# Performance work log

Measured on AMD Instinct MI355X. Metric: run time of the kernel, lower is better.

The kernel has to match this reference:

```python
import jax, jax.numpy as jnp
import numpy as np

T, S, B, D, H, DH, DI = 1024, 1024, 4, 1024, 16, 64, 4096
SCALE = 1.0 / (DH ** 0.5)


def _ln(x, g, b, eps=1e-5):
    m = jnp.mean(x, axis=-1, keepdims=True)
    v = jnp.mean((x - m) ** 2, axis=-1, keepdims=True)
    return (x - m) * jax.lax.rsqrt(v + eps) * g + b


def setup_inputs() -> dict:
    key = jax.random.key(0)
    ks = jax.random.split(key, 16)
    s = 0.02
    inp = {
        "dec_inp": jax.random.normal(ks[0], (T, B, D), jnp.float32),
        "enc_out": jax.random.normal(ks[1], (T, B, D), jnp.float32),
        # causal mask for self-attn: [qlen, klen, bsz], True = masked
        "dec_mask": jnp.broadcast_to(jnp.triu(jnp.ones((T, T), bool), 1)[:, :, None], (T, T, B)),
        # encoder padding mask: [klen, bsz], last 128 positions padded
        "enc_mask": jnp.broadcast_to((jnp.arange(S) >= S - 128)[:, None], (S, B)),
        # self-attn params
        "W_q1": jax.random.normal(ks[2], (D, H * DH), jnp.float32) * s,
        "W_kv1": jax.random.normal(ks[3], (D, 2 * H * DH), jnp.float32) * s,
        "W_o1": jax.random.normal(ks[4], (H * DH, D), jnp.float32) * s,
        "g1": jnp.ones((D,), jnp.float32), "b1": jnp.zeros((D,), jnp.float32),
        # cross-attn params
        "W_q2": jax.random.normal(ks[5], (D, H * DH), jnp.float32) * s,
        "W_kv2": jax.random.normal(ks[6], (D, 2 * H * DH), jnp.float32) * s,
        "W_o2": jax.random.normal(ks[7], (H * DH, D), jnp.float32) * s,
        "g2": jnp.ones((D,), jnp.float32), "b2": jnp.zeros((D,), jnp.float32),
        # FFN params
        "W_ff1": jax.random.normal(ks[8], (D, DI), jnp.float32) * s,
        "b_ff1": jnp.zeros((DI,), jnp.float32),
        "W_ff2": jax.random.normal(ks[9], (DI, D), jnp.float32) * s,
        "b_ff2": jnp.zeros((D,), jnp.float32),
        "g3": jnp.ones((D,), jnp.float32), "b3": jnp.zeros((D,), jnp.float32),
    }
    return inp


def reference(dec_inp, enc_out, dec_mask, enc_mask,
              W_q1, W_kv1, W_o1, g1, b1,
              W_q2, W_kv2, W_o2, g2, b2,
              W_ff1, b_ff1, W_ff2, b_ff2, g3, b3):
    # ---- self-attention (MultiHeadAttn, pre_lnorm=True, mems=None) ----
    # NOTE: q is computed from the UN-normalized h; k,v from LN(c) — faithful to source.
    c = _ln(dec_inp, g1, b1)
    q = (dec_inp @ W_q1).reshape(T, B, H, DH)
    kv = (c @ W_kv1)
    k, v = jnp.split(kv, 2, axis=-1)
    k = k.reshape(T, B, H, DH)
    v = v.reshape(T, B, H, DH)
    score = jnp.einsum('ibnd,jbnd->ijbn', q, k) * SCALE  # [T,T,B,H]
    score = jnp.where(dec_mask[:, :, :, None], -jnp.inf, score)
    prob = jax.nn.softmax(score, axis=1)
    vec = jnp.einsum('ijbn,jbnd->ibnd', prob, v).reshape(T, B, H * DH)
    out1 = dec_inp + vec @ W_o1

    # ---- cross-attention (ContextMultiHeadAttn, pre_lnorm=True) ----
    # NOTE: residual uses the layer-normed h (source reassigns h = layer_norm(h)).
    h2 = _ln(out1, g2, b2)
    q2 = (h2 @ W_q2).reshape(T, B, H, DH)
    kv2 = enc_out @ W_kv2  # enc_out is NOT layer-normed in source
    k2, v2 = jnp.split(kv2, 2, axis=-1)
    k2 = k2.reshape(S, B, H, DH)
    v2 = v2.reshape(S, B, H, DH)
    score2 = jnp.einsum('ibnd,jbnd->ijbn', q2, k2) * SCALE  # [T,S,B,H]
    score2 = jnp.where(enc_mask[None, :, :, None], -10000.0, score2)
    prob2 = jax.nn.softmax(score2, axis=1)
    vec2 = jnp.einsum('ijbn,jbnd->ibnd', prob2, v2).reshape(T, B, H * DH)
    out2 = h2 + vec2 @ W_o2

    # ---- position-wise FFN (pre_lnorm) ----
    h3 = _ln(out2, g3, b3)
    core = jax.nn.gelu(h3 @ W_ff1 + b_ff1, approximate=False) @ W_ff2 + b_ff2
    return out2 + core
```

## Files before the change

kernel.cpp:

```cpp
#include <hip/hip_runtime.h>
#include <hip/hip_bf16.h>

#define T_ 1024
#define S_ 1024
#define B_ 4
#define D_ 1024
#define H_ 16
#define DH_ 64
#define DI_ 4096
#define NTOK 4096

typedef __attribute__((ext_vector_type(8))) short bf16x8;
typedef __attribute__((ext_vector_type(4))) float f32x4;

__device__ __forceinline__ short f2bf(float f) {
  unsigned u = __builtin_bit_cast(unsigned, f);
  u += 0x7fffu + ((u >> 16) & 1u);
  return (short)(u >> 16);
}

__device__ __forceinline__ void g2l16(const void* g, void* l) {
  __builtin_amdgcn_global_load_lds(
      (const __attribute__((address_space(1))) unsigned int*)g,
      (__attribute__((address_space(3))) unsigned int*)l, 16, 0, 0);
}

__device__ __forceinline__ void bar() {
  asm volatile("" ::: "memory");
  __builtin_amdgcn_s_barrier();
  asm volatile("" ::: "memory");
}

__device__ __forceinline__ void xcd_swz(int& bx, int& by) {
  const int gx = gridDim.x;
  const int id0 = blockIdx.y * gx + blockIdx.x;
  const int cpx = (gx * gridDim.y) >> 3;
  const int nid = (id0 & 7) * cpx + (id0 >> 3);
  bx = nid % gx;
  by = nid / gx;
}

template <int EPI>
__global__ __launch_bounds__(512, 2) void gemm8p(
    const short* __restrict__ A, const short* __restrict__ Bt,
    float* __restrict__ outF, short* __restrict__ outB,
    const float* __restrict__ res, const float* __restrict__ bias,
    int M, int N, int K) {
  __shared__ short sA[2][256 * 64];
  __shared__ short sB[2][256 * 64];
  const int tid = threadIdx.x;
  const int lane = tid & 63;
  const int w = tid >> 6;
  const int wm = w >> 2, wn = w & 3;
  const int r15 = lane & 15, g4 = lane >> 4;
  int bx, by;
  xcd_swz(bx, by);
  const size_t row0 = (size_t)bx * 256;
  const size_t col0 = (size_t)by * 256;

  f32x4 acc[8][4];
#pragma unroll
  for (int i = 0; i < 8; i++)
#pragma unroll
    for (int j = 0; j < 4; j++) acc[i][j] = (f32x4){0.f, 0.f, 0.f, 0.f};

  auto stageA = [&](int buf, int s, int kt) {
    const int k0 = kt << 6;
#pragma unroll
    for (int j = 0; j < 2; ++j) {
      const int c = j * 8 + w;
      const int rb = ((c >> 3) << 7) + (s << 6) + ((c & 7) << 3);
      const int row = rb + (lane >> 3);
      const int col = k0 + (((lane & 7) ^ (row & 7)) << 3);
      g2l16(A + (row0 + row) * (size_t)K + col, &sA[buf][rb * 64]);
    }
  };
  auto stageB = [&](int buf, int s, int kt) {
    const int k0 = kt << 6;
#pragma unroll
    for (int j = 0; j < 2; ++j) {
      const int c = j * 8 + w;
      const int rb = ((c >> 2) << 6) + (s << 5) + ((c & 3) << 3);
      const int row = rb + (lane >> 3);
      const int col = k0 + (((lane & 7) ^ (row & 7)) << 3);
      g2l16(Bt + (col0 + row) * (size_t)K + col, &sB[buf][rb * 64]);
    }
  };

  const int nk = K >> 6;
  stageA(0, 0, 0); stageA(0, 1, 0); stageB(0, 0, 0); stageB(0, 1, 0);
  if (nk > 1) {
    stageA(1, 0, 1); stageB(1, 1, 1);
    asm volatile("s_waitcnt vmcnt(4)" ::: "memory");
  } else {
    asm volatile("s_waitcnt vmcnt(0)" ::: "memory");
  }
  bar();

  bf16x8 af[4][2], bv[2][2];
  for (int t = 0; t < nk; ++t) {
    const int cur = t & 1;
    const short* cA = sA[cur];
    const short* cB = sB[cur];
#pragma unroll
    for (int mi = 0; mi < 4; mi++) {
      const int rowA = wm * 128 + mi * 16 + r15;
#pragma unroll
      for (int kk = 0; kk < 2; kk++)
        af[mi][kk] = *(const bf16x8*)(cA + rowA * 64 +
                                      (((kk * 4 + g4) ^ (rowA & 7)) << 3));
    }
#pragma unroll
    for (int ni = 0; ni < 2; ni++) {
      const int rowB = wn * 64 + ni * 16 + r15;
#pragma unroll
      for (int kk = 0; kk < 2; kk++)
        bv[ni][kk] = *(const bf16x8*)(cB + rowB * 64 +
                                      (((kk * 4 + g4) ^ (rowB & 7)) << 3));
    }
    if (t + 1 < nk) stageA(cur ^ 1, 1, t + 1);
    bar();
    asm volatile("s_waitcnt lgkmcnt(0)" ::: "memory");
    __builtin_amdgcn_s_setprio(1);
#pragma unroll
    for (int kk = 0; kk < 2; kk++)
#pragma unroll
      for (int mi = 0; mi < 4; mi++)
#pragma unroll
        for (int ni = 0; ni < 2; ni++)
          acc[mi][ni] = __builtin_amdgcn_mfma_f32_16x16x32_bf16(
              af[mi][kk], bv[ni][kk], acc[mi][ni], 0, 0, 0);
    __builtin_amdgcn_s_setprio(0);
    bar();
#pragma unroll
    for (int ni = 0; ni < 2; ni++) {
      const int rowB = wn * 64 + (2 + ni) * 16 + r15;
#pragma unroll
      for (int kk = 0; kk < 2; kk++)
        bv[ni][kk] = *(const bf16x8*)(cB + rowB * 64 +
                                      (((kk * 4 + g4) ^ (rowB & 7)) << 3));
    }
    if (t + 1 < nk) stageB(cur ^ 1, 0, t + 1);
    bar();
    asm volatile("s_waitcnt lgkmcnt(0)" ::: "memory");
    __builtin_amdgcn_s_setprio(1);
#pragma unroll
    for (int kk = 0; kk < 2; kk++)
#pragma unroll
      for (int mi = 0; mi < 4; mi++)
#pragma unroll
        for (int ni = 0; ni < 2; ni++)
          acc[mi][2 + ni] = __builtin_amdgcn_mfma_f32_16x16x32_bf16(
              af[mi][kk], bv[ni][kk], acc[mi][2 + ni], 0, 0, 0);
    __builtin_amdgcn_s_setprio(0);
    bar();
#pragma unroll
    for (int mi = 0; mi < 4; mi++) {
      const int rowA = wm * 128 + (4 + mi) * 16 + r15;
#pragma unroll
      for (int kk = 0; kk < 2; kk++)
        af[mi][kk] = *(const bf16x8*)(cA + rowA * 64 +
                                      (((kk * 4 + g4) ^ (rowA & 7)) << 3));
    }
    if (t + 2 < nk) stageA(cur, 0, t + 2);
    bar();
    asm volatile("s_waitcnt lgkmcnt(0)" ::: "memory");
    __builtin_amdgcn_s_setprio(1);
#pragma unroll
    for (int kk = 0; kk < 2; kk++)
#pragma unroll
      for (int mi = 0; mi < 4; mi++)
#pragma unroll
        for (int ni = 0; ni < 2; ni++)
          acc[4 + mi][2 + ni] = __builtin_amdgcn_mfma_f32_16x16x32_bf16(
              af[mi][kk], bv[ni][kk], acc[4 + mi][2 + ni], 0, 0, 0);
    __builtin_amdgcn_s_setprio(0);
    bar();
#pragma unroll
    for (int ni = 0; ni < 2; ni++) {
      const int rowB = wn * 64 + ni * 16 + r15;
#pragma unroll
      for (int kk = 0; kk < 2; kk++)
        bv[ni][kk] = *(const bf16x8*)(cB + rowB * 64 +
                                      (((kk * 4 + g4) ^ (rowB & 7)) << 3));
    }
    if (t + 2 < nk) stageB(cur, 1, t + 2);
    bar();
    asm volatile("s_waitcnt lgkmcnt(0)" ::: "memory");
    __builtin_amdgcn_s_setprio(1);
#pragma unroll
    for (int kk = 0; kk < 2; kk++)
#pragma unroll
      for (int mi = 0; mi < 4; mi++)
#pragma unroll
        for (int ni = 0; ni < 2; ni++)
          acc[4 + mi][ni] = __builtin_amdgcn_mfma_f32_16x16x32_bf16(
              af[mi][kk], bv[ni][kk], acc[4 + mi][ni], 0, 0, 0);
    __builtin_amdgcn_s_setprio(0);
    if (t + 2 < nk)
      asm volatile("s_waitcnt vmcnt(4)" ::: "memory");
    else if (t + 1 < nk)
      asm volatile("s_waitcnt vmcnt(0)" ::: "memory");
    bar();
  }

#pragma unroll
  for (int mi = 0; mi < 8; mi++) {
    size_t row = row0 + wm * 128 + mi * 16 + (g4 << 2);
#pragma unroll
    for (int ni = 0; ni < 4; ni++) {
      size_t col = col0 + wn * 64 + ni * 16 + r15;
      float bcol = (EPI == 2 || EPI == 3) ? bias[col] : 0.f;
#pragma unroll
      for (int r = 0; r < 4; r++) {
        size_t idx = (row + r) * (size_t)N + col;
        float v = acc[mi][ni][r];
        if (EPI == 0) {
          outB[idx] = f2bf(v);
        } else if (EPI == 1) {
          outF[idx] = v + res[idx];
        } else if (EPI == 2) {
          float x = v + bcol;
          float gl = 0.5f * x * (1.f + erff(x * 0.70710678118654752f));
          outB[idx] = f2bf(gl);
        } else {
          outF[idx] = v + bcol + res[idx];
        }
      }
    }
  }
}

template <int EPI, int BN>
__global__ __launch_bounds__(256, 2) void gemm_bt(
    const short* __restrict__ A, const short* __restrict__ Bt,
    float* __restrict__ outF, short* __restrict__ outB,
    const float* __restrict__ res, const float* __restrict__ bias,
    short* __restrict__ Kgp, short* __restrict__ Vgp,
    int M, int N, int K) {
  constexpr int WCOLS = BN / 64;
  constexpr int MI = (WCOLS == 2) ? 4 : 2;
  constexpr int BLOADS = BN / 32;
  __shared__ short sA[2][128 * 64];
  __shared__ short sB[2][BN * 64];
  const int tid = threadIdx.x;
  const int lane = tid & 63;
  const int w = tid >> 6;
  const int wr = (WCOLS == 2) ? (w >> 1) : w;
  const int wc = (WCOLS == 2) ? (w & 1) : 0;
  const int r15 = lane & 15, g4 = lane >> 4;
  int bx, by;
  xcd_swz(bx, by);
  const size_t row0 = (size_t)bx * 128;
  const size_t col0 = (size_t)by * BN;

  f32x4 acc[MI][4];
#pragma unroll
  for (int i = 0; i < MI; i++)
#pragma unroll
    for (int j = 0; j < 4; j++) acc[i][j] = (f32x4){0.f, 0.f, 0.f, 0.f};

  auto stage = [&](int buf, int kt) {
    const int k0 = kt << 6;
#pragma unroll
    for (int i = 0; i < 4; i++) {
      int flat = i * 256 + tid;
      int row = flat >> 3;
      int col = k0 + (((flat & 7) ^ (row & 7)) << 3);
      g2l16(A + (row0 + row) * (size_t)K + col, &sA[buf][(i * 256 + w * 64) * 8]);
    }
#pragma unroll
    for (int i = 0; i < BLOADS; i++) {
      int flat = i * 256 + tid;
      int row = flat >> 3;
      int col = k0 + (((flat & 7) ^ (row & 7)) << 3);
      g2l16(Bt + (col0 + row) * (size_t)K + col, &sB[buf][(i * 256 + w * 64) * 8]);
    }
  };

  stage(0, 0);
  __syncthreads();

  const int nk = K >> 6;
  for (int kt = 0; kt < nk; ++kt) {
    const int cur = kt & 1;
    if (kt + 1 < nk) stage(cur ^ 1, kt + 1);
#pragma unroll
    for (int kk = 0; kk < 2; ++kk) {
      bf16x8 af[MI], bfr[4];
#pragma unroll
      for (int mi = 0; mi < MI; mi++) {
        int rowA = wr * (MI * 16) + mi * 16 + r15;
        af[mi] = *(const bf16x8*)(&sA[cur][rowA * 64 +
                                           (((kk * 4 + g4) ^ (rowA & 7)) << 3)]);
      }
#pragma unroll
      for (int ni = 0; ni < 4; ni++) {
        int rowB = wc * 64 + ni * 16 + r15;
        bfr[ni] = *(const bf16x8*)(&sB[cur][rowB * 64 +
                                            (((kk * 4 + g4) ^ (rowB & 7)) << 3)]);
      }
#pragma unroll
      for (int mi = 0; mi < MI; mi++)
#pragma unroll
        for (int ni = 0; ni < 4; ni++)
          acc[mi][ni] = __builtin_amdgcn_mfma_f32_16x16x32_bf16(af[mi], bfr[ni],
                                                                acc[mi][ni], 0, 0, 0);
    }
    __syncthreads();
  }

#pragma unroll
  for (int mi = 0; mi < MI; mi++) {
    size_t row = row0 + wr * (MI * 16) + mi * 16 + (g4 << 2);
#pragma unroll
    for (int ni = 0; ni < 4; ni++) {
      size_t col = col0 + wc * 64 + ni * 16 + r15;
      float bcol = (EPI == 2 || EPI == 3) ? bias[col] : 0.f;
#pragma unroll
      for (int r = 0; r < 4; r++) {
        size_t idx = (row + r) * (size_t)N + col;
        float v = acc[mi][ni][r];
        if (EPI == 0) {
          outB[idx] = f2bf(v);
        } else if (EPI == 1) {
          outF[idx] = v + res[idx];
        } else if (EPI == 2) {
          float x = v + bcol;
          float gl = 0.5f * x * (1.f + erff(x * 0.70710678118654752f));
          outB[idx] = f2bf(gl);
        } else if (EPI == 3) {
          outF[idx] = v + bcol + res[idx];
        } else {
          int tt = (int)(row + r) >> 2;
          int bb = (int)(row + r) & 3;
          int cc = (int)col;
          if (cc < 1024) {
            int hh = cc >> 6, dd = cc & 63;
            size_t base = (size_t)(bb * 16 + hh) * 65536 + (size_t)tt * 64;
            Kgp[base + ((((dd >> 3) ^ (tt & 7)) << 3) | (dd & 7))] = f2bf(v * 0.125f);
          } else {
            int hh = (cc >> 6) - 16, dd = cc & 63;
            int k6 = tt & 63;
            int kap = ((k6 & 15) << 2) | (k6 >> 4);
            size_t base = (size_t)(bb * 16 + hh) * 65536 + (size_t)(tt >> 6) * 4096;
            Vgp[base + (kap >> 3) * 512 + dd * 8 + (kap & 7)] = f2bf(v);
          }
        }
      }
    }
  }
}

template <int MODE>
__global__ __launch_bounds__(256, 3) void attn_k2(const short* __restrict__ Qm,
                                                  const short* __restrict__ Kg,
                                                  const short* __restrict__ Vg,
                                                  short* __restrict__ Om) {
  __shared__ short Kl[2][4096];
  __shared__ short Vl[2][4096];
  __shared__ short Pl[4][2048];
  const int tid = threadIdx.x;
  const int lane = tid & 63;
  const int w = tid >> 6;
  const int r15 = lane & 15, g4 = lane >> 4;
  const int bh = blockIdx.x;
  const int qt = blockIdx.y;
  const int b = bh >> 4, h = bh & 15;
  const int qbase = qt * 128 + w * 32;
  const int ktDiag = qbase >> 6;

  bf16x8 qf[2][2];
#pragma unroll
  for (int g = 0; g < 2; g++)
#pragma unroll
    for (int hf = 0; hf < 2; hf++) {
      int row = qbase + g * 16 + r15;
      qf[g][hf] = *(const bf16x8*)(Qm + ((size_t)(row * 4 + b)) * 1024 + h * 64 +
                                   hf * 32 + g4 * 8);
    }

  const size_t kvbase = (size_t)bh * 65536;
  const int nkt = (MODE == 0) ? (2 * qt + 2) : 14;

  f32x4 o[2][4];
#pragma unroll
  for (int g = 0; g < 2; g++)
#pragma unroll
    for (int ni = 0; ni < 4; ni++) o[g][ni] = (f32x4){0.f, 0.f, 0.f, 0.f};
  float mrun[2][4], lrun[2][4];
#pragma unroll
  for (int g = 0; g < 2; g++)
#pragma unroll
    for (int r = 0; r < 4; r++) { mrun[g][r] = -1e30f; lrun[g][r] = 0.f; }

  {
    const size_t tb = kvbase;
#pragma unroll
    for (int i = 0; i < 2; i++) {
      g2l16(Kg + tb + (size_t)(i * 256 + tid) * 8, &Kl[0][(i * 256 + w * 64) * 8]);
      g2l16(Vg + tb + (size_t)(i * 256 + tid) * 8, &Vl[0][(i * 256 + w * 64) * 8]);
    }
  }
  __syncthreads();

  for (int kt = 0; kt < nkt; kt++) {
    const int cur = kt & 1;
    if (kt + 1 < nkt) {
      const size_t tb = kvbase + (size_t)(kt + 1) * 4096;
#pragma unroll
      for (int i = 0; i < 2; i++) {
        g2l16(Kg + tb + (size_t)(i * 256 + tid) * 8,
              &Kl[cur ^ 1][(i * 256 + w * 64) * 8]);
        g2l16(Vg + tb + (size_t)(i * 256 + tid) * 8,
              &Vl[cur ^ 1][(i * 256 + w * 64) * 8]);
      }
    }

    const bool active = (MODE == 1) || (kt * 64 <= qbase + 31);
    if (active) {
      bf16x8 kb[4][2];
#pragma unroll
      for (int ni = 0; ni < 4; ni++) {
        int row = ni * 16 + r15;
        kb[ni][0] = *(const bf16x8*)(&Kl[cur][row * 64 + ((g4 ^ (row & 7)) << 3)]);
        kb[ni][1] =
            *(const bf16x8*)(&Kl[cur][row * 64 + (((g4 + 4) ^ (row & 7)) << 3)]);
      }
      f32x4 sf[2][4];
#pragma unroll
      for (int g = 0; g < 2; g++)
#pragma unroll
        for (int ni = 0; ni < 4; ni++) {
          f32x4 s = (f32x4){0.f, 0.f, 0.f, 0.f};
          s = __builtin_amdgcn_mfma_f32_16x16x32_bf16(qf[g][0], kb[ni][0], s, 0, 0, 0);
          s = __builtin_amdgcn_mfma_f32_16x16x32_bf16(qf[g][1], kb[ni][1], s, 0, 0, 0);
          sf[g][ni] = s;
        }
      if (MODE == 0 && kt >= ktDiag) {
#pragma unroll
        for (int g = 0; g < 2; g++)
#pragma unroll
          for (int ni = 0; ni < 4; ni++)
#pragma unroll
            for (int r = 0; r < 4; r++) {
              int q = qbase + g * 16 + g4 * 4 + r;
              int key = kt * 64 + ni * 16 + r15;
              if (key > q) sf[g][ni][r] = -1e30f;
            }
      }
#pragma unroll
      for (int g = 0; g < 2; g++) {
        float corr[4];
#pragma unroll
        for (int r = 0; r < 4; r++) {
          float m = fmaxf(fmaxf(sf[g][0][r], sf[g][1][r]),
                          fmaxf(sf[g][2][r], sf[g][3][r]));
          m = fmaxf(m, __shfl_xor(m, 1));
          m = fmaxf(m, __shfl_xor(m, 2));
          m = fmaxf(m, __shfl_xor(m, 4));
          m = fmaxf(m, __shfl_xor(m, 8));
          float mn = fmaxf(mrun[g][r], m);
          corr[r] = __expf(mrun[g][r] - mn);
          mrun[g][r] = mn;
        }
        float rs[4] = {0.f, 0.f, 0.f, 0.f};
#pragma unroll
        for (int ni = 0; ni < 4; ni++)
#pragma unroll
          for (int r = 0; r < 4; r++) {
            float p = __expf(sf[g][ni][r] - mrun[g][r]);
            sf[g][ni][r] = p;
            rs[r] += p;
          }
#pragma unroll
        for (int r = 0; r < 4; r++) {
          rs[r] += __shfl_xor(rs[r], 1);
          rs[r] += __shfl_xor(rs[r], 2);
          rs[r] += __shfl_xor(rs[r], 4);
          rs[r] += __shfl_xor(rs[r], 8);
          lrun[g][r] = lrun[g][r] * corr[r] + rs[r];
        }
#pragma unroll
        for (int ni = 0; ni < 4; ni++)
#pragma unroll
          for (int r = 0; r < 4; r++) o[g][ni][r] *= corr[r];
#pragma unroll
        for (int r = 0; r < 4; r++) {
          int qr = g * 16 + g4 * 4 + r;
          short4 pk;
          pk.x = f2bf(sf[g][0][r]);
          pk.y = f2bf(sf[g][1][r]);
          pk.z = f2bf(sf[g][2][r]);
          pk.w = f2bf(sf[g][3][r]);
          int gran = (r15 >> 1) ^ (qr & 7);
          *(short4*)(&Pl[w][qr * 64 + gran * 8 + (r15 & 1) * 4]) = pk;
        }
      }
#pragma unroll
      for (int kk = 0; kk < 2; kk++) {
        int gw = kk * 4 + g4;
        bf16x8 pa0 = *(const bf16x8*)(&Pl[w][r15 * 64 + ((gw ^ (r15 & 7)) << 3)]);
        bf16x8 pa1 =
            *(const bf16x8*)(&Pl[w][(16 + r15) * 64 + ((gw ^ (r15 & 7)) << 3)]);
#pragma unroll
        for (int ni = 0; ni < 4; ni++) {
          bf16x8 vb = *(const bf16x8*)(&Vl[cur][(gw * 64 + ni * 16 + r15) * 8]);
          o[0][ni] = __builtin_amdgcn_mfma_f32_16x16x32_bf16(pa0, vb, o[0][ni], 0, 0, 0);
          o[1][ni] = __builtin_amdgcn_mfma_f32_16x16x32_bf16(pa1, vb, o[1][ni], 0, 0, 0);
        }
      }
    }
    __syncthreads();
  }

#pragma unroll
  for (int g = 0; g < 2; g++) {
    float inv[4];
#pragma unroll
    for (int r = 0; r < 4; r++) inv[r] = 1.f / lrun[g][r];
#pragma unroll
    for (int ni = 0; ni < 4; ni++) {
      int col = h * 64 + ni * 16 + r15;
#pragma unroll
      for (int r = 0; r < 4; r++) {
        int tg = qbase + g * 16 + g4 * 4 + r;
        Om[((size_t)(tg * 4 + b)) * 1024 + col] = f2bf(o[g][ni][r] * inv[r]);
      }
    }
  }
}

__global__ __launch_bounds__(256) void ln_k(const float* __restrict__ x,
                                            const float* __restrict__ gw,
                                            const float* __restrict__ bw,
                                            float* __restrict__ outF,
                                            short* __restrict__ outB,
                                            short* __restrict__ outXB) {
  const int row = blockIdx.x, tid = threadIdx.x;
  const float4 v = ((const float4*)(x + (size_t)row * 1024))[tid];
  float s = v.x + v.y + v.z + v.w;
  float ss = v.x * v.x + v.y * v.y + v.z * v.z + v.w * v.w;
#pragma unroll
  for (int d = 32; d >= 1; d >>= 1) {
    s += __shfl_xor(s, d);
    ss += __shfl_xor(ss, d);
  }
  __shared__ float red[8];
  const int w = tid >> 6;
  if ((tid & 63) == 0) { red[w] = s; red[4 + w] = ss; }
  __syncthreads();
  s = red[0] + red[1] + red[2] + red[3];
  ss = red[4] + red[5] + red[6] + red[7];
  const float mean = s * (1.f / 1024.f);
  const float var = ss * (1.f / 1024.f) - mean * mean;
  const float rstd = rsqrtf(var + 1e-5f);
  const float4 gv = ((const float4*)gw)[tid];
  const float4 bv = ((const float4*)bw)[tid];
  float4 y;
  y.x = (v.x - mean) * rstd * gv.x + bv.x;
  y.y = (v.y - mean) * rstd * gv.y + bv.y;
  y.z = (v.z - mean) * rstd * gv.z + bv.z;
  y.w = (v.w - mean) * rstd * gv.w + bv.w;
  if (outF) ((float4*)(outF + (size_t)row * 1024))[tid] = y;
  if (outB) {
    short4 ob;
    ob.x = f2bf(y.x); ob.y = f2bf(y.y); ob.z = f2bf(y.z); ob.w = f2bf(y.w);
    ((short4*)(outB + (size_t)row * 1024))[tid] = ob;
  }
  if (outXB) {
    short4 ob;
    ob.x = f2bf(v.x); ob.y = f2bf(v.y); ob.z = f2bf(v.z); ob.w = f2bf(v.w);
    ((short4*)(outXB + (size_t)row * 1024))[tid] = ob;
  }
}

__global__ __launch_bounds__(256) void cvt_bf16(const float* __restrict__ in,
                                                short* __restrict__ out) {
  const size_t i = (size_t)blockIdx.x * 256 + threadIdx.x;
  const float4 v = ((const float4*)in)[i];
  short4 ob;
  ob.x = f2bf(v.x); ob.y = f2bf(v.y); ob.z = f2bf(v.z); ob.w = f2bf(v.w);
  ((short4*)out)[i] = ob;
}

__global__ __launch_bounds__(256) void tr_cvt(const float* __restrict__ in,
                                              short* __restrict__ out, int K, int N) {
  __shared__ float t[64][65];
  const int tid = threadIdx.x;
  const int k0 = blockIdx.x * 64, n0 = blockIdx.y * 64;
#pragma unroll
  for (int i = 0; i < 16; i++) {
    int flat = i * 256 + tid;
    int r = flat >> 6, c = flat & 63;
    t[r][c] = in[(size_t)(k0 + r) * N + n0 + c];
  }
  __syncthreads();
#pragma unroll
  for (int i = 0; i < 16; i++) {
    int flat = i * 256 + tid;
    int r = flat >> 6, c = flat & 63;
    out[(size_t)(n0 + r) * K + k0 + c] = f2bf(t[c][r]);
  }
}

extern "C" void kernel_launch(void* const* d_in, const int* in_sizes, int n_in,
                              void* d_out, int out_size, void* d_ws, size_t ws_size,
                              hipStream_t stream) {
  const float* dec_inp = (const float*)d_in[0];
  const float* enc_out = (const float*)d_in[1];
  const float* W_q1 = (const float*)d_in[4];
  const float* W_kv1 = (const float*)d_in[5];
  const float* W_o1 = (const float*)d_in[6];
  const float* g1 = (const float*)d_in[7];
  const float* b1 = (const float*)d_in[8];
  const float* W_q2 = (const float*)d_in[9];
  const float* W_kv2 = (const float*)d_in[10];
  const float* W_o2 = (const float*)d_in[11];
  const float* g2 = (const float*)d_in[12];
  const float* b2 = (const float*)d_in[13];
  const float* W_ff1 = (const float*)d_in[14];
  const float* b_ff1 = (const float*)d_in[15];
  const float* W_ff2 = (const float*)d_in[16];
  const float* b_ff2 = (const float*)d_in[17];
  const float* g3 = (const float*)d_in[18];
  const float* b3 = (const float*)d_in[19];
  float* out = (float*)d_out;

  char* ws = (char*)d_ws;
  size_t off = 0;
  auto alloc = [&](size_t bytes) -> void* {
    void* p = ws + off;
    off += (bytes + 255) & ~(size_t)255;
    return p;
  };
  short* Wq1t = (short*)alloc(1024ull * 1024 * 2);
  short* Wkv1t = (short*)alloc(2048ull * 1024 * 2);
  short* Wo1t = (short*)alloc(1024ull * 1024 * 2);
  short* Wq2t = (short*)alloc(1024ull * 1024 * 2);
  short* Wkv2t = (short*)alloc(2048ull * 1024 * 2);
  short* Wo2t = (short*)alloc(1024ull * 1024 * 2);
  short* Wff1t = (short*)alloc(4096ull * 1024 * 2);
  short* Wff2t = (short*)alloc(1024ull * 4096 * 2);
  short* Xbf = (short*)alloc((size_t)NTOK * 1024 * 2);
  short* Ebf = (short*)alloc((size_t)NTOK * 1024 * 2);
  short* Cbf = (short*)alloc((size_t)NTOK * 1024 * 2);
  short* Qb = (short*)alloc((size_t)NTOK * 1024 * 2);
  short* Kg = (short*)alloc(64ull * 65536 * 2);
  short* Vg = (short*)alloc(64ull * 65536 * 2);
  short* VECb = (short*)alloc((size_t)NTOK * 1024 * 2);
  float* OUT1 = (float*)alloc((size_t)NTOK * 1024 * 4);
  float* H2f = (float*)alloc((size_t)NTOK * 1024 * 4);
  float* OUT2 = (float*)alloc((size_t)NTOK * 1024 * 4);
  short* FF1 = (short*)alloc((size_t)NTOK * 4096 * 2);
  short* H2b = Xbf;
  short* H3b = Cbf;

  dim3 blk(256, 1, 1);

  tr_cvt<<<dim3(16, 16), blk, 0, stream>>>(W_q1, Wq1t, 1024, 1024);
  tr_cvt<<<dim3(16, 32), blk, 0, stream>>>(W_kv1, Wkv1t, 1024, 2048);
  tr_cvt<<<dim3(16, 16), blk, 0, stream>>>(W_o1, Wo1t, 1024, 1024);
  tr_cvt<<<dim3(16, 16), blk, 0, stream>>>(W_q2, Wq2t, 1024, 1024);
  tr_cvt<<<dim3(16, 32), blk, 0, stream>>>(W_kv2, Wkv2t, 1024, 2048);
  tr_cvt<<<dim3(16, 16), blk, 0, stream>>>(W_o2, Wo2t, 1024, 1024);
  tr_cvt<<<dim3(16, 64), blk, 0, stream>>>(W_ff1, Wff1t, 1024, 4096);
  tr_cvt<<<dim3(64, 16), blk, 0, stream>>>(W_ff2, Wff2t, 4096, 1024);

  cvt_bf16<<<4096, blk, 0, stream>>>(enc_out, Ebf);
  ln_k<<<4096, blk, 0, stream>>>(dec_inp, g1, b1, nullptr, Cbf, Xbf);

  gemm_bt<0, 64><<<dim3(32, 16), blk, 0, stream>>>(
      Xbf, Wq1t, nullptr, Qb, nullptr, nullptr, nullptr, nullptr, 4096, 1024, 1024);
  gemm_bt<4, 128><<<dim3(32, 16), blk, 0, stream>>>(
      Cbf, Wkv1t, nullptr, nullptr, nullptr, nullptr, Kg, Vg, 4096, 2048, 1024);
  attn_k2<0><<<dim3(64, 8), blk, 0, stream>>>(Qb, Kg, Vg, VECb);
  gemm_bt<1, 64><<<dim3(32, 16), blk, 0, stream>>>(
      VECb, Wo1t, OUT1, nullptr, dec_inp, nullptr, nullptr, nullptr, 4096, 1024, 1024);
  ln_k<<<4096, blk, 0, stream>>>(OUT1, g2, b2, H2f, H2b, nullptr);
  gemm_bt<0, 64><<<dim3(32, 16), blk, 0, stream>>>(
      H2b, Wq2t, nullptr, Qb, nullptr, nullptr, nullptr, nullptr, 4096, 1024, 1024);
  gemm_bt<4, 128><<<dim3(32, 16), blk, 0, stream>>>(
      Ebf, Wkv2t, nullptr, nullptr, nullptr, nullptr, Kg, Vg, 4096, 2048, 1024);
  attn_k2<1><<<dim3(64, 8), blk, 0, stream>>>(Qb, Kg, Vg, VECb);
  gemm_bt<1, 64><<<dim3(32, 16), blk, 0, stream>>>(
      VECb, Wo2t, OUT2, nullptr, H2f, nullptr, nullptr, nullptr, 4096, 1024, 1024);
  ln_k<<<4096, blk, 0, stream>>>(OUT2, g3, b3, nullptr, H3b, nullptr);
  gemm8p<2><<<dim3(16, 16), dim3(512, 1, 1), 0, stream>>>(
      H3b, Wff1t, nullptr, FF1, nullptr, b_ff1, 4096, 4096, 1024);
  gemm_bt<3, 64><<<dim3(32, 16), blk, 0, stream>>>(
      FF1, Wff2t, out, nullptr, OUT2, b_ff2, nullptr, nullptr, 4096, 1024, 4096);
}
```

Measured before the change: 399.3 us.

## Triple-buffer gemm_bt with single barrier, drop XCD swizzle and BN=128 variant

Rewrites the gemm_bt main loop to a three-stage LDS ring: it prefetches two tiles ahead and uses explicit vmcnt waits with one barrier per k-step instead of two syncthreads. This is meant to hide global-to-LDS latency better. It also removes the XCD block-index swizzle from both GEMM kernels and replaces the BN=128 KV-projection tiles with BN=64 on a doubled grid. Dropping the swizzle can hurt L2 locality across XCDs, and the smaller KV tile reduces reuse of A.

```diff
diff --git a/kernel.cpp b/kernel.cpp
--- a/kernel.cpp
+++ b/kernel.cpp
@@ -29,15 +29,6 @@
   asm volatile("" ::: "memory");
   __builtin_amdgcn_s_barrier();
   asm volatile("" ::: "memory");
-}
-
-__device__ __forceinline__ void xcd_swz(int& bx, int& by) {
-  const int gx = gridDim.x;
-  const int id0 = blockIdx.y * gx + blockIdx.x;
-  const int cpx = (gx * gridDim.y) >> 3;
-  const int nid = (id0 & 7) * cpx + (id0 >> 3);
-  bx = nid % gx;
-  by = nid / gx;
 }
 
 template <int EPI>
@@ -53,10 +44,8 @@
   const int w = tid >> 6;
   const int wm = w >> 2, wn = w & 3;
   const int r15 = lane & 15, g4 = lane >> 4;
-  int bx, by;
-  xcd_swz(bx, by);
-  const size_t row0 = (size_t)bx * 256;
-  const size_t col0 = (size_t)by * 256;
+  const size_t row0 = (size_t)blockIdx.x * 256;
+  const size_t col0 = (size_t)blockIdx.y * 256;
 
   f32x4 acc[8][4];
 #pragma unroll
@@ -231,32 +220,25 @@
   }
 }
 
-template <int EPI, int BN>
+template <int EPI>
 __global__ __launch_bounds__(256, 2) void gemm_bt(
     const short* __restrict__ A, const short* __restrict__ Bt,
     float* __restrict__ outF, short* __restrict__ outB,
     const float* __restrict__ res, const float* __restrict__ bias,
     short* __restrict__ Kgp, short* __restrict__ Vgp,
     int M, int N, int K) {
-  constexpr int WCOLS = BN / 64;
-  constexpr int MI = (WCOLS == 2) ? 4 : 2;
-  constexpr int BLOADS = BN / 32;
-  __shared__ short sA[2][128 * 64];
-  __shared__ short sB[2][BN * 64];
+  __shared__ short sA[3][128 * 64];
+  __shared__ short sB[3][64 * 64];
   const int tid = threadIdx.x;
   const int lane = tid & 63;
   const int w = tid >> 6;
-  const int wr = (WCOLS == 2) ? (w >> 1) : w;
-  const int wc = (WCOLS == 2) ? (w & 1) : 0;
   const int r15 = lane & 15, g4 = lane >> 4;
-  int bx, by;
-  xcd_swz(bx, by);
-  const size_t row0 = (size_t)bx * 128;
-  const size_t col0 = (size_t)by * BN;
-
-  f32x4 acc[MI][4];
-#pragma unroll
-  for (int i = 0; i < MI; i++)
+  const size_t row0 = (size_t)blockIdx.x * 128;
+  const size_t col0 = (size_t)blockIdx.y * 64;
+
+  f32x4 acc[2][4];
+#pragma unroll
+  for (int i = 0; i < 2; i++)
 #pragma unroll
     for (int j = 0; j < 4; j++) acc[i][j] = (f32x4){0.f, 0.f, 0.f, 0.f};
 
@@ -270,7 +252,7 @@
       g2l16(A + (row0 + row) * (size_t)K + col, &sA[buf][(i * 256 + w * 64) * 8]);
     }
 #pragma unroll
-    for (int i = 0; i < BLOADS; i++) {
+    for (int i = 0; i < 2; i++) {
       int flat = i * 256 + tid;
       int row = flat >> 3;
       int col = k0 + (((flat & 7) ^ (row & 7)) << 3);
@@ -278,44 +260,54 @@
     }
   };
 
+  const int nk = K >> 6;
   stage(0, 0);
-  __syncthreads();
-
-  const int nk = K >> 6;
+  stage(1, 1);
+  int cur = 0;
   for (int kt = 0; kt < nk; ++kt) {
-    const int cur = kt & 1;
-    if (kt + 1 < nk) stage(cur ^ 1, kt + 1);
+    if (kt + 1 < nk)
+      asm volatile("s_waitcnt vmcnt(6)" ::: "memory");
+    else
+      asm volatile("s_waitcnt vmcnt(0)" ::: "memory");
+    bar();
+    if (kt + 2 < nk) {
+      int nxt = cur + 2;
+      if (nxt >= 3) nxt -= 3;
+      stage(nxt, kt + 2);
+    }
+    const short* cA = sA[cur];
+    const short* cB = sB[cur];
 #pragma unroll
     for (int kk = 0; kk < 2; ++kk) {
-      bf16x8 af[MI], bfr[4];
-#pragma unroll
-      for (int mi = 0; mi < MI; mi++) {
-        int rowA = wr * (MI * 16) + mi * 16 + r15;
-        af[mi] = *(const bf16x8*)(&sA[cur][rowA * 64 +
-                                           (((kk * 4 + g4) ^ (rowA & 7)) << 3)]);
+      bf16x8 af[2], bfr[4];
+#pragma unroll
+      for (int mi = 0; mi < 2; mi++) {
+        int rowA = w * 32 + mi * 16 + r15;
+        af[mi] = *(const bf16x8*)(cA + rowA * 64 +
+                                  (((kk * 4 + g4) ^ (rowA & 7)) << 3));
       }
 #pragma unroll
       for (int ni = 0; ni < 4; ni++) {
-        int rowB = wc * 64 + ni * 16 + r15;
-        bfr[ni] = *(const bf16x8*)(&sB[cur][rowB * 64 +
-                                            (((kk * 4 + g4) ^ (rowB & 7)) << 3)]);
-      }
-#pragma unroll
-      for (int mi = 0; mi < MI; mi++)
+        int rowB = ni * 16 + r15;
+        bfr[ni] = *(const bf16x8*)(cB + rowB * 64 +
+                                   (((kk * 4 + g4) ^ (rowB & 7)) << 3));
+      }
+#pragma unroll
+      for (int mi = 0; mi < 2; mi++)
 #pragma unroll
         for (int ni = 0; ni < 4; ni++)
           acc[mi][ni] = __builtin_amdgcn_mfma_f32_16x16x32_bf16(af[mi], bfr[ni],
                                                                 acc[mi][ni], 0, 0, 0);
     }
-    __syncthreads();
-  }
-
-#pragma unroll
-  for (int mi = 0; mi < MI; mi++) {
-    size_t row = row0 + wr * (MI * 16) + mi * 16 + (g4 << 2);
+    cur = (cur == 2) ? 0 : cur + 1;
+  }
+
+#pragma unroll
+  for (int mi = 0; mi < 2; mi++) {
+    size_t row = row0 + w * 32 + mi * 16 + (g4 << 2);
 #pragma unroll
     for (int ni = 0; ni < 4; ni++) {
-      size_t col = col0 + wc * 64 + ni * 16 + r15;
+      size_t col = col0 + ni * 16 + r15;
       float bcol = (EPI == 2 || EPI == 3) ? bias[col] : 0.f;
 #pragma unroll
       for (int r = 0; r < 4; r++) {
@@ -670,24 +662,24 @@
   cvt_bf16<<<4096, blk, 0, stream>>>(enc_out, Ebf);
   ln_k<<<4096, blk, 0, stream>>>(dec_inp, g1, b1, nullptr, Cbf, Xbf);
 
-  gemm_bt<0, 64><<<dim3(32, 16), blk, 0, stream>>>(
+  gemm_bt<0><<<dim3(32, 16), blk, 0, stream>>>(
       Xbf, Wq1t, nullptr, Qb, nullptr, nullptr, nullptr, nullptr, 4096, 1024, 1024);
-  gemm_bt<4, 128><<<dim3(32, 16), blk, 0, stream>>>(
+  gemm_bt<4><<<dim3(32, 32), blk, 0, stream>>>(
       Cbf, Wkv1t, nullptr, nullptr, nullptr, nullptr, Kg, Vg, 4096, 2048, 1024);
   attn_k2<0><<<dim3(64, 8), blk, 0, stream>>>(Qb, Kg, Vg, VECb);
-  gemm_bt<1, 64><<<dim3(32, 16), blk, 0, stream>>>(
+  gemm_bt<1><<<dim3(32, 16), blk, 0, stream>>>(
       VECb, Wo1t, OUT1, nullptr, dec_inp, nullptr, nullptr, nullptr, 4096, 1024, 1024);
   ln_k<<<4096, blk, 0, stream>>>(OUT1, g2, b2, H2f, H2b, nullptr);
-  gemm_bt<0, 64><<<dim3(32, 16), blk, 0, stream>>>(
+  gemm_bt<0><<<dim3(32, 16), blk, 0, stream>>>(
       H2b, Wq2t, nullptr, Qb, nullptr, nullptr, nullptr, nullptr, 4096, 1024, 1024);
-  gemm_bt<4, 128><<<dim3(32, 16), blk, 0, stream>>>(
+  gemm_bt<4><<<dim3(32, 32), blk, 0, stream>>>(
       Ebf, Wkv2t, nullptr, nullptr, nullptr, nullptr, Kg, Vg, 4096, 2048, 1024);
   attn_k2<1><<<dim3(64, 8), blk, 0, stream>>>(Qb, Kg, Vg, VECb);
-  gemm_bt<1, 64><<<dim3(32, 16), blk, 0, stream>>>(
+  gemm_bt<1><<<dim3(32, 16), blk, 0, stream>>>(
       VECb, Wo2t, OUT2, nullptr, H2f, nullptr, nullptr, nullptr, 4096, 1024, 1024);
   ln_k<<<4096, blk, 0, stream>>>(OUT2, g3, b3, nullptr, H3b, nullptr);
   gemm8p<2><<<dim3(16, 16), dim3(512, 1, 1), 0, stream>>>(
       H3b, Wff1t, nullptr, FF1, nullptr, b_ff1, 4096, 4096, 1024);
-  gemm_bt<3, 64><<<dim3(32, 16), blk, 0, stream>>>(
+  gemm_bt<3><<<dim3(32, 16), blk, 0, stream>>>(
       FF1, Wff2t, out, nullptr, OUT2, b_ff2, nullptr, nullptr, 4096, 1024, 4096);
 }
```

Result: no change. 398.9 us (-0.1%).
